# Performance work log

Hardware: AMD Instinct MI355X
Metric: run time of the kernel (lower is better)

## Reference

```python
import jax, jax.numpy as jnp
import numpy as np

D = 1024
H = 16
DH = D // H
FF = 4096
EPS = 1e-6


def setup_inputs() -> dict:
    key = jax.random.key(0)
    ks = jax.random.split(key, 8)
    s = 1.0 / np.sqrt(D)
    return {
        "x": jax.random.normal(ks[0], (2, 2048, D), jnp.float32),
        # attention projections stored [in, out] (math equals torch Linear x @ W.T)
        "w_q": jax.random.normal(ks[1], (D, D), jnp.float32) * s,
        "w_k": jax.random.normal(ks[2], (D, D), jnp.float32) * s,
        "w_v": jax.random.normal(ks[3], (D, D), jnp.float32) * s,
        "w_o": jax.random.normal(ks[4], (D, D), jnp.float32) * s,
        "w1": jax.random.normal(ks[5], (D, FF), jnp.float32) * s,
        "b1": jnp.zeros((FF,), jnp.float32),
        "w2": jax.random.normal(ks[6], (FF, D), jnp.float32) * (1.0 / np.sqrt(FF)),
        "b2": jnp.zeros((D,), jnp.float32),
        "g1": jnp.ones((D,), jnp.float32),
        "be1": jnp.zeros((D,), jnp.float32),
        "g2": jnp.ones((D,), jnp.float32),
        "be2": jnp.zeros((D,), jnp.float32),
    }


def _layernorm(x, gamma, beta):
    # torch .std() uses Bessel correction (ddof=1); note std+eps, not var+eps
    mean = jnp.mean(x, axis=-1, keepdims=True)
    std = jnp.std(x, axis=-1, keepdims=True, ddof=1)
    return gamma * (x - mean) / (std + EPS) + beta


def _attention(h, w_q, w_k, w_v, w_o):
    B, S, _ = h.shape
    q = (h @ w_q).reshape(B, S, H, DH)
    k = (h @ w_k).reshape(B, S, H, DH)
    v = (h @ w_v).reshape(B, S, H, DH)
    scores = jnp.einsum('bqhd,bkhd->bhqk', q, k) / np.sqrt(DH)  # [B,H,S,S]
    attn = jax.nn.softmax(scores, axis=-1)
    out = jnp.einsum('bhqk,bkhd->bqhd', attn, v).reshape(B, S, D)
    return out @ w_o


def reference(x, w_q, w_k, w_v, w_o, w1, b1, w2, b2, g1, be1, g2, be2):
    # pre-norm residual 1: self-attention (dropout=0 / eval)
    x = x + _attention(_layernorm(x, g1, be1), w_q, w_k, w_v, w_o)
    # pre-norm residual 2: FFN
    h = _layernorm(x, g2, be2)
    x = x + (jax.nn.relu(h @ w1 + b1) @ w2 + b2)
    return x
```

## Files before the change

### kernel.cpp

```cpp
#include <hip/hip_runtime.h>


typedef _Float16 half8 __attribute__((ext_vector_type(8)));
typedef _Float16 half4 __attribute__((ext_vector_type(4)));
typedef float floatx4 __attribute__((ext_vector_type(4)));

__device__ __forceinline__ void async16(const void* g, void* l) {
    __builtin_amdgcn_global_load_lds((const __attribute__((address_space(1))) unsigned int*)g,
                                     (__attribute__((address_space(3))) unsigned int*)l,
                                     16, 0, 0);
}

__global__ __launch_bounds__(256) void ln_kernel(const float* __restrict__ x,
                                                 const float* __restrict__ g,
                                                 const float* __restrict__ be,
                                                 _Float16* __restrict__ out) {
    int row = blockIdx.x;
    int tid = threadIdx.x;
    floatx4 v = ((const floatx4*)(x + (size_t)row * 1024))[tid];
    float s = 0.f, ss = 0.f;
#pragma unroll
    for (int i = 0; i < 4; i++) { s += v[i]; ss += v[i] * v[i]; }
#pragma unroll
    for (int off = 1; off < 64; off <<= 1) {
        s += __shfl_xor(s, off);
        ss += __shfl_xor(ss, off);
    }
    __shared__ float sm[8];
    int wave = tid >> 6, lane = tid & 63;
    if (lane == 0) { sm[wave] = s; sm[wave + 4] = ss; }
    __syncthreads();
    s = sm[0] + sm[1] + sm[2] + sm[3];
    ss = sm[4] + sm[5] + sm[6] + sm[7];
    float mean = s * (1.f / 1024.f);
    float var = (ss - s * mean) * (1.f / 1023.f);
    float rs = 1.f / (sqrtf(fmaxf(var, 0.f)) + 1e-6f);
    floatx4 gv = ((const floatx4*)g)[tid];
    floatx4 bv = ((const floatx4*)be)[tid];
    half4 o;
#pragma unroll
    for (int i = 0; i < 4; i++) o[i] = (_Float16)(gv[i] * (v[i] - mean) * rs + bv[i]);
    ((half4*)(out + (size_t)row * 1024))[tid] = o;
}

__global__ __launch_bounds__(256) void convt_kernel(const float* __restrict__ W, int ldW,
                                                    _Float16* __restrict__ WT, int Kr,
                                                    float scale) {
    __shared__ float t[64][65];
    int n0 = blockIdx.x * 64, k0 = blockIdx.y * 64;
    int tid = threadIdx.x;
    int r = tid >> 4, c4 = (tid & 15) * 4;
#pragma unroll
    for (int p = 0; p < 4; p++) {
        floatx4 v = *(const floatx4*)(W + (size_t)(k0 + r + p * 16) * ldW + n0 + c4);
#pragma unroll
        for (int j = 0; j < 4; j++) t[c4 + j][r + p * 16] = v[j];
    }
    __syncthreads();
#pragma unroll
    for (int p = 0; p < 4; p++) {
        int rr = r + p * 16;
        half4 o;
#pragma unroll
        for (int j = 0; j < 4; j++) o[j] = (_Float16)(t[rr][c4 + j] * scale);
        *(half4*)(WT + (size_t)(n0 + rr) * Kr + k0 + c4) = o;
    }
}

__global__ __launch_bounds__(256) void transv_kernel(const _Float16* __restrict__ V, int ldv,
                                                     _Float16* __restrict__ Vt) {
    __shared__ _Float16 t[64][72];
    int t0 = blockIdx.x * 64, d0 = blockIdx.y * 64;
    int tid = threadIdx.x;
#pragma unroll
    for (int i = 0; i < 2; i++) {
        int v = tid + i * 256;
        int r = v >> 3, c = (v & 7) * 8;
        half8 vv = *(const half8*)(V + (size_t)(t0 + r) * ldv + d0 + c);
#pragma unroll
        for (int j = 0; j < 8; j++) t[c + j][r] = vv[j];
    }
    __syncthreads();
    int bh = (t0 >> 11) * 16 + (d0 >> 6);
    int sbase = t0 & 2047;
#pragma unroll
    for (int i = 0; i < 2; i++) {
        int v = tid + i * 256;
        int r = v >> 3, c = (v & 7) * 8;
        half8 o = *(const half8*)&t[r][c];
        *(half8*)(Vt + ((size_t)bh * 64 + r) * 2048 + sbase + c) = o;
    }
}

__global__ __launch_bounds__(256) void gemm_t(const _Float16* __restrict__ A, int lda,
                                              const _Float16* __restrict__ BT,
                                              const float* __restrict__ bias,
                                              const float* res, void* Cout,
                                              int N, int K, int relu_flag, int out_fp16) {
    __shared__ _Float16 As[64 * 64];
    __shared__ _Float16 Bs[128 * 64];
    int tid = threadIdx.x;
    int wave = tid >> 6, lane = tid & 63, quad = lane >> 4, l15 = lane & 15;
    int bm = blockIdx.y * 64, bn = blockIdx.x * 128;
    int wr = (wave & 1) * 32, wc = (wave >> 1) * 64;
    int lrow = lane >> 3, lch = lane & 7;

    floatx4 acc[2][4];
#pragma unroll
    for (int im = 0; im < 2; im++)
#pragma unroll
        for (int in = 0; in < 4; in++)
#pragma unroll
            for (int r = 0; r < 4; r++) acc[im][in][r] = 0.f;

    for (int k0 = 0; k0 < K; k0 += 64) {
        __syncthreads();
#pragma unroll
        for (int ia = 0; ia < 2; ia++) {
            int g = 2 * wave + ia;
            int row = g * 8 + lrow;
            int ch = lch ^ (row & 7);
            async16(A + (size_t)(bm + row) * lda + k0 + ch * 8, &As[g * 512]);
        }
#pragma unroll
        for (int ib = 0; ib < 4; ib++) {
            int g = 4 * wave + ib;
            int row = g * 8 + lrow;
            int ch = lch ^ (row & 7);
            async16(BT + (size_t)(bn + row) * K + k0 + ch * 8, &Bs[g * 512]);
        }
        __syncthreads();

        half8 af[2][2], bf[4][2];
#pragma unroll
        for (int kk = 0; kk < 2; kk++) {
#pragma unroll
            for (int im = 0; im < 2; im++) {
                int m = wr + im * 16 + l15;
                af[im][kk] = *(const half8*)&As[m * 64 + ((((kk << 2) | quad) ^ (m & 7)) << 3)];
            }
#pragma unroll
            for (int in = 0; in < 4; in++) {
                int n = wc + in * 16 + l15;
                bf[in][kk] = *(const half8*)&Bs[n * 64 + ((((kk << 2) | quad) ^ (n & 7)) << 3)];
            }
        }
#pragma unroll
        for (int kk = 0; kk < 2; kk++)
#pragma unroll
            for (int im = 0; im < 2; im++)
#pragma unroll
                for (int in = 0; in < 4; in++)
                    acc[im][in] = __builtin_amdgcn_mfma_f32_16x16x32_f16(af[im][kk], bf[in][kk],
                                                                         acc[im][in], 0, 0, 0);
    }
#pragma unroll
    for (int im = 0; im < 2; im++)
#pragma unroll
        for (int in = 0; in < 4; in++)
#pragma unroll
            for (int r = 0; r < 4; r++) {
                int row = bm + wr + im * 16 + quad * 4 + r;
                int col = bn + wc + in * 16 + l15;
                float val = acc[im][in][r];
                if (bias) val += bias[col];
                if (relu_flag) val = fmaxf(val, 0.f);
                if (res) val += res[(size_t)row * N + col];
                if (out_fp16) ((_Float16*)Cout)[(size_t)row * N + col] = (_Float16)val;
                else          ((float*)Cout)[(size_t)row * N + col] = val;
            }
}

__global__ __launch_bounds__(256) void attn_kernel(const _Float16* Q,
                                                   const _Float16* __restrict__ K,
                                                   const _Float16* __restrict__ Vt,
                                                   _Float16* O, int ld) {
    __shared__ _Float16 Qs[64 * 64];
    __shared__ _Float16 KVs[2][2][64 * 64];
    int qt = blockIdx.x, bh = blockIdx.y;
    int b = bh >> 4, h = bh & 15;
    int col0 = h * 64, tbase = b * 2048;
    int tid = threadIdx.x;
    int wave = tid >> 6, lane = tid & 63, quad = lane >> 4, l15 = lane & 15;
    int lrow = lane >> 3, lch = lane & 7;

#pragma unroll
    for (int i = 0; i < 2; i++) {
        int g = 2 * wave + i;
        int row = g * 8 + lrow;
        int ch = lch ^ (row & 7);
        async16(Q + (size_t)(tbase + qt * 64 + row) * ld + col0 + ch * 8, &Qs[g * 512]);
        async16(K + (size_t)(tbase + row) * ld + col0 + ch * 8, &KVs[0][0][g * 512]);
        async16(Vt + ((size_t)bh * 64 + row) * 2048 + ch * 8, &KVs[0][1][g * 512]);
    }
    __syncthreads();

    int rowq = 16 * wave + l15;
    half8 bq[2];
#pragma unroll
    for (int kk = 0; kk < 2; kk++)
        bq[kk] = *(const half8*)&Qs[rowq * 64 + ((((kk << 2) | quad) ^ (rowq & 7)) << 3)];

    floatx4 o_acc[4];
#pragma unroll
    for (int im = 0; im < 4; im++)
#pragma unroll
        for (int r = 0; r < 4; r++) o_acc[im][r] = 0.f;
    float m_i = -1e30f, l_i = 0.f;

    for (int kt = 0; kt < 32; kt++) {
        if (kt) __syncthreads();
        if (kt + 1 < 32) {
            int nb = (kt + 1) & 1;
#pragma unroll
            for (int i = 0; i < 2; i++) {
                int g = 2 * wave + i;
                int row = g * 8 + lrow;
                int ch = lch ^ (row & 7);
                async16(K + (size_t)(tbase + (kt + 1) * 64 + row) * ld + col0 + ch * 8,
                        &KVs[nb][0][g * 512]);
                async16(Vt + ((size_t)bh * 64 + row) * 2048 + (kt + 1) * 64 + ch * 8,
                        &KVs[nb][1][g * 512]);
            }
        }
        const _Float16* Ks = KVs[kt & 1][0];
        const _Float16* Vs = KVs[kt & 1][1];

        floatx4 s_acc[4];
#pragma unroll
        for (int jn = 0; jn < 4; jn++)
#pragma unroll
            for (int r = 0; r < 4; r++) s_acc[jn][r] = 0.f;
#pragma unroll
        for (int jn = 0; jn < 4; jn++) {
            int rowk = 16 * jn + l15;
#pragma unroll
            for (int kk = 0; kk < 2; kk++) {
                half8 ak = *(const half8*)&Ks[rowk * 64 + ((((kk << 2) | quad) ^ (rowk & 7)) << 3)];
                s_acc[jn] = __builtin_amdgcn_mfma_f32_16x16x32_f16(ak, bq[kk], s_acc[jn], 0, 0, 0);
            }
        }

        float mx = -1e30f;
#pragma unroll
        for (int jn = 0; jn < 4; jn++)
#pragma unroll
            for (int r = 0; r < 4; r++) mx = fmaxf(mx, s_acc[jn][r]);
        mx = fmaxf(mx, __shfl_xor(mx, 16));
        mx = fmaxf(mx, __shfl_xor(mx, 32));
        float mnew = fmaxf(m_i, mx);
        float dd = m_i - mnew;
        float alpha = (dd < -60.f) ? 0.f : __expf(dd);
        m_i = mnew;

        float sum = 0.f;
#pragma unroll
        for (int jn = 0; jn < 4; jn++)
#pragma unroll
            for (int r = 0; r < 4; r++) {
                float d2 = s_acc[jn][r] - mnew;
                float p = (d2 < -60.f) ? 0.f : __expf(d2);
                s_acc[jn][r] = p;
                sum += p;
            }
        sum += __shfl_xor(sum, 16);
        sum += __shfl_xor(sum, 32);
        l_i = l_i * alpha + sum;

        half4 pb[4];
#pragma unroll
        for (int jn = 0; jn < 4; jn++)
#pragma unroll
            for (int r = 0; r < 4; r++) pb[jn][r] = (_Float16)s_acc[jn][r];

#pragma unroll
        for (int im = 0; im < 4; im++)
#pragma unroll
            for (int r = 0; r < 4; r++) o_acc[im][r] *= alpha;
#pragma unroll
        for (int im = 0; im < 4; im++) {
            int rowv = 16 * im + l15;
#pragma unroll
            for (int ks = 0; ks < 4; ks++) {
                int off = rowv * 128 + ((((2 * ks) | (quad >> 1)) ^ (rowv & 7)) << 4) + (quad & 1) * 8;
                half4 av = *(const half4*)((const char*)Vs + off);
                o_acc[im] = __builtin_amdgcn_mfma_f32_16x16x16f16(av, pb[ks], o_acc[im], 0, 0, 0);
            }
        }
    }

    float rl = 1.f / l_i;
#pragma unroll
    for (int im = 0; im < 4; im++) {
        half4 o;
#pragma unroll
        for (int r = 0; r < 4; r++) o[r] = (_Float16)(o_acc[im][r] * rl);
        *(half4*)&O[(size_t)(tbase + qt * 64 + wave * 16 + l15) * ld + col0 + im * 16 + quad * 4] = o;
    }
}

extern "C" void kernel_launch(void* const* d_in, const int* in_sizes, int n_in,
                              void* d_out, int out_size, void* d_ws, size_t ws_size,
                              hipStream_t stream) {
    const float* x   = (const float*)d_in[0];
    const float* wq  = (const float*)d_in[1];
    const float* wk  = (const float*)d_in[2];
    const float* wv  = (const float*)d_in[3];
    const float* wo  = (const float*)d_in[4];
    const float* w1  = (const float*)d_in[5];
    const float* b1  = (const float*)d_in[6];
    const float* w2  = (const float*)d_in[7];
    const float* b2  = (const float*)d_in[8];
    const float* g1  = (const float*)d_in[9];
    const float* be1 = (const float*)d_in[10];
    const float* g2  = (const float*)d_in[11];
    const float* be2 = (const float*)d_in[12];

    const size_t M1 = (size_t)1 << 20;
    _Float16* R0  = (_Float16*)d_ws;
    _Float16* QKV = R0 + 4 * M1;
    _Float16* R3  = R0 + 12 * M1;

    _Float16* wqkvT = (_Float16*)d_out;
    float* x1 = (float*)d_out;
    float* out = (float*)d_out;

    dim3 blk(256);

    convt_kernel<<<dim3(16, 16), blk, 0, stream>>>(wq, 1024, wqkvT, 1024, 0.125f);
    convt_kernel<<<dim3(16, 16), blk, 0, stream>>>(wk, 1024, wqkvT + (size_t)1024 * 1024, 1024, 1.f);
    convt_kernel<<<dim3(16, 16), blk, 0, stream>>>(wv, 1024, wqkvT + (size_t)2048 * 1024, 1024, 1.f);
    ln_kernel<<<4096, blk, 0, stream>>>(x, g1, be1, R0);
    gemm_t<<<dim3(24, 64), blk, 0, stream>>>(R0, 1024, wqkvT, nullptr, nullptr, QKV, 3072, 1024, 0, 1);
    transv_kernel<<<dim3(64, 16), blk, 0, stream>>>(QKV + 2048, 3072, R0);
    attn_kernel<<<dim3(32, 32), blk, 0, stream>>>(QKV, QKV + 1024, R0, QKV, 3072);
    convt_kernel<<<dim3(16, 16), blk, 0, stream>>>(wo, 1024, R0, 1024, 1.f);
    gemm_t<<<dim3(8, 64), blk, 0, stream>>>(QKV, 3072, R0, nullptr, x, x1, 1024, 1024, 0, 0);
    ln_kernel<<<4096, blk, 0, stream>>>(x1, g2, be2, R0);
    _Float16* f = QKV;
    for (int hh = 0; hh < 2; hh++) {
        _Float16* w1Th = R3;
        _Float16* w2Th = R3 + 2 * M1;
        convt_kernel<<<dim3(32, 16), blk, 0, stream>>>(w1 + hh * 2048, 4096, w1Th, 1024, 1.f);
        gemm_t<<<dim3(16, 64), blk, 0, stream>>>(R0, 1024, w1Th, b1 + hh * 2048, nullptr, f,
                                                 2048, 1024, 1, 1);
        convt_kernel<<<dim3(16, 32), blk, 0, stream>>>(w2 + (size_t)hh * 2048 * 1024, 1024, w2Th, 2048, 1.f);
        gemm_t<<<dim3(8, 64), blk, 0, stream>>>(f, 2048, w2Th, (hh == 1) ? b2 : nullptr, x1, out,
                                                1024, 2048, 0, 0);
    }
}
```

Measured before the change: 452.1 us.

## Add 128x128 GEMM tile for QKV/FFN1 and lazy-rescale online softmax in attention

Adds a gemm_t128 kernel with 128x128 output tiles (4x4 MFMA fragments per wave) and uses it for the QKV projection and the first FFN GEMM, raising arithmetic intensity per loaded tile. In attention, the running max is updated only when any lane's block max exceeds the current max by more than 8, which skips the rescale of O and l most of the time. Exponentials switch to exp2 with a folded log2e, and conversion uses packed round-toward-zero fp16. The new GEMM is single-buffered with more registers and fewer blocks, which may cost occupancy. The lazy max allows p values up to e^8, which fits in fp16 but loses a little precision.

```diff
diff --git a/kernel.cpp b/kernel.cpp
--- a/kernel.cpp
+++ b/kernel.cpp
@@ -3,6 +3,7 @@
 
 typedef _Float16 half8 __attribute__((ext_vector_type(8)));
 typedef _Float16 half4 __attribute__((ext_vector_type(4)));
+typedef __fp16 fp16x2 __attribute__((ext_vector_type(2)));
 typedef float floatx4 __attribute__((ext_vector_type(4)));
 
 __device__ __forceinline__ void async16(const void* g, void* l) {
@@ -171,6 +172,85 @@
             }
 }
 
+__global__ __launch_bounds__(256) void gemm_t128(const _Float16* __restrict__ A, int lda,
+                                                 const _Float16* __restrict__ BT,
+                                                 const float* __restrict__ bias,
+                                                 const float* res, void* Cout,
+                                                 int N, int K, int relu_flag, int out_fp16) {
+    __shared__ _Float16 As[128 * 64];
+    __shared__ _Float16 Bs[128 * 64];
+    int tid = threadIdx.x;
+    int wave = tid >> 6, lane = tid & 63, quad = lane >> 4, l15 = lane & 15;
+    int bm = blockIdx.y * 128, bn = blockIdx.x * 128;
+    int wr = (wave & 1) * 64, wc = (wave >> 1) * 64;
+    int lrow = lane >> 3, lch = lane & 7;
+
+    floatx4 acc[4][4];
+#pragma unroll
+    for (int im = 0; im < 4; im++)
+#pragma unroll
+        for (int in = 0; in < 4; in++)
+#pragma unroll
+            for (int r = 0; r < 4; r++) acc[im][in][r] = 0.f;
+
+    for (int k0 = 0; k0 < K; k0 += 64) {
+        __syncthreads();
+#pragma unroll
+        for (int ia = 0; ia < 4; ia++) {
+            int g = 4 * wave + ia;
+            int row = g * 8 + lrow;
+            int ch = lch ^ (row & 7);
+            async16(A + (size_t)(bm + row) * lda + k0 + ch * 8, &As[g * 512]);
+        }
+#pragma unroll
+        for (int ib = 0; ib < 4; ib++) {
+            int g = 4 * wave + ib;
+            int row = g * 8 + lrow;
+            int ch = lch ^ (row & 7);
+            async16(BT + (size_t)(bn + row) * K + k0 + ch * 8, &Bs[g * 512]);
+        }
+        __syncthreads();
+
+        half8 af[4][2], bf[4][2];
+#pragma unroll
+        for (int kk = 0; kk < 2; kk++) {
+#pragma unroll
+            for (int im = 0; im < 4; im++) {
+                int m = wr + im * 16 + l15;
+                af[im][kk] = *(const half8*)&As[m * 64 + ((((kk << 2) | quad) ^ (m & 7)) << 3)];
+            }
+#pragma unroll
+            for (int in = 0; in < 4; in++) {
+                int n = wc + in * 16 + l15;
+                bf[in][kk] = *(const half8*)&Bs[n * 64 + ((((kk << 2) | quad) ^ (n & 7)) << 3)];
+            }
+        }
+#pragma unroll
+        for (int kk = 0; kk < 2; kk++)
+#pragma unroll
+            for (int im = 0; im < 4; im++)
+#pragma unroll
+                for (int in = 0; in < 4; in++)
+                    acc[im][in] = __builtin_amdgcn_mfma_f32_16x16x32_f16(af[im][kk], bf[in][kk],
+                                                                         acc[im][in], 0, 0, 0);
+    }
+#pragma unroll
+    for (int im = 0; im < 4; im++)
+#pragma unroll
+        for (int in = 0; in < 4; in++)
+#pragma unroll
+            for (int r = 0; r < 4; r++) {
+                int row = bm + wr + im * 16 + quad * 4 + r;
+                int col = bn + wc + in * 16 + l15;
+                float val = acc[im][in][r];
+                if (bias) val += bias[col];
+                if (relu_flag) val = fmaxf(val, 0.f);
+                if (res) val += res[(size_t)row * N + col];
+                if (out_fp16) ((_Float16*)Cout)[(size_t)row * N + col] = (_Float16)val;
+                else          ((float*)Cout)[(size_t)row * N + col] = val;
+            }
+}
+
 __global__ __launch_bounds__(256) void attn_kernel(const _Float16* Q,
                                                    const _Float16* __restrict__ K,
                                                    const _Float16* __restrict__ Vt,
@@ -207,6 +287,7 @@
 #pragma unroll
         for (int r = 0; r < 4; r++) o_acc[im][r] = 0.f;
     float m_i = -1e30f, l_i = 0.f;
+    const float LOG2E = 1.44269504f;
 
     for (int kt = 0; kt < 32; kt++) {
         if (kt) __syncthreads();
@@ -248,35 +329,37 @@
             for (int r = 0; r < 4; r++) mx = fmaxf(mx, s_acc[jn][r]);
         mx = fmaxf(mx, __shfl_xor(mx, 16));
         mx = fmaxf(mx, __shfl_xor(mx, 32));
-        float mnew = fmaxf(m_i, mx);
-        float dd = m_i - mnew;
-        float alpha = (dd < -60.f) ? 0.f : __expf(dd);
-        m_i = mnew;
+        if (!__all(mx <= m_i + 8.f)) {
+            float mnew = fmaxf(m_i, mx);
+            float dd = m_i - mnew;
+            float alpha = (dd < -60.f) ? 0.f : __expf(dd);
+            l_i *= alpha;
+#pragma unroll
+            for (int im = 0; im < 4; im++)
+#pragma unroll
+                for (int r = 0; r < 4; r++) o_acc[im][r] *= alpha;
+            m_i = mnew;
+        }
+        float m2 = m_i * LOG2E;
 
         float sum = 0.f;
-#pragma unroll
-        for (int jn = 0; jn < 4; jn++)
-#pragma unroll
-            for (int r = 0; r < 4; r++) {
-                float d2 = s_acc[jn][r] - mnew;
-                float p = (d2 < -60.f) ? 0.f : __expf(d2);
-                s_acc[jn][r] = p;
-                sum += p;
-            }
+        half4 pb[4];
+#pragma unroll
+        for (int jn = 0; jn < 4; jn++) {
+            float p0 = exp2f(fmaf(s_acc[jn][0], LOG2E, -m2));
+            float p1 = exp2f(fmaf(s_acc[jn][1], LOG2E, -m2));
+            float p2 = exp2f(fmaf(s_acc[jn][2], LOG2E, -m2));
+            float p3 = exp2f(fmaf(s_acc[jn][3], LOG2E, -m2));
+            sum += (p0 + p1) + (p2 + p3);
+            fp16x2 lo = __builtin_amdgcn_cvt_pkrtz(p0, p1);
+            fp16x2 hi = __builtin_amdgcn_cvt_pkrtz(p2, p3);
+            pb[jn][0] = (_Float16)lo[0]; pb[jn][1] = (_Float16)lo[1];
+            pb[jn][2] = (_Float16)hi[0]; pb[jn][3] = (_Float16)hi[1];
+        }
         sum += __shfl_xor(sum, 16);
         sum += __shfl_xor(sum, 32);
-        l_i = l_i * alpha + sum;
-
-        half4 pb[4];
-#pragma unroll
-        for (int jn = 0; jn < 4; jn++)
-#pragma unroll
-            for (int r = 0; r < 4; r++) pb[jn][r] = (_Float16)s_acc[jn][r];
-
-#pragma unroll
-        for (int im = 0; im < 4; im++)
-#pragma unroll
-            for (int r = 0; r < 4; r++) o_acc[im][r] *= alpha;
+        l_i += sum;
+
 #pragma unroll
         for (int im = 0; im < 4; im++) {
             int rowv = 16 * im + l15;
@@ -331,7 +414,7 @@
     convt_kernel<<<dim3(16, 16), blk, 0, stream>>>(wk, 1024, wqkvT + (size_t)1024 * 1024, 1024, 1.f);
     convt_kernel<<<dim3(16, 16), blk, 0, stream>>>(wv, 1024, wqkvT + (size_t)2048 * 1024, 1024, 1.f);
     ln_kernel<<<4096, blk, 0, stream>>>(x, g1, be1, R0);
-    gemm_t<<<dim3(24, 64), blk, 0, stream>>>(R0, 1024, wqkvT, nullptr, nullptr, QKV, 3072, 1024, 0, 1);
+    gemm_t128<<<dim3(24, 32), blk, 0, stream>>>(R0, 1024, wqkvT, nullptr, nullptr, QKV, 3072, 1024, 0, 1);
     transv_kernel<<<dim3(64, 16), blk, 0, stream>>>(QKV + 2048, 3072, R0);
     attn_kernel<<<dim3(32, 32), blk, 0, stream>>>(QKV, QKV + 1024, R0, QKV, 3072);
     convt_kernel<<<dim3(16, 16), blk, 0, stream>>>(wo, 1024, R0, 1024, 1.f);
@@ -342,8 +425,8 @@
         _Float16* w1Th = R3;
         _Float16* w2Th = R3 + 2 * M1;
         convt_kernel<<<dim3(32, 16), blk, 0, stream>>>(w1 + hh * 2048, 4096, w1Th, 1024, 1.f);
-        gemm_t<<<dim3(16, 64), blk, 0, stream>>>(R0, 1024, w1Th, b1 + hh * 2048, nullptr, f,
-                                                 2048, 1024, 1, 1);
+        gemm_t128<<<dim3(16, 32), blk, 0, stream>>>(R0, 1024, w1Th, b1 + hh * 2048, nullptr, f,
+                                                    2048, 1024, 1, 1);
         convt_kernel<<<dim3(16, 32), blk, 0, stream>>>(w2 + (size_t)hh * 2048 * 1024, 1024, w2Th, 2048, 1.f);
         gemm_t<<<dim3(8, 64), blk, 0, stream>>>(f, 2048, w2Th, (hh == 1) ? b2 : nullptr, x1, out,
                                                 1024, 2048, 0, 0);
```

Measured after the change: 461.5 us. +2.1%, slower.

## Unroll attention loop by two with precomputed LDS pointers and lazy rescaling

Applied to the files above, without the earlier changes.

Restructures the flash-attention inner loop into a two-step unrolled body with compile-time buffer indices, precomputed LDS fragment pointers and incrementing global pointers, to cut per-iteration address arithmetic. It also adds a lazy online-softmax rescale that skips the alpha correction unless the max grows by more than a threshold, uses exp2 with a fused log2e scale, and packs fp16 conversion with cvt_pkrtz. Keeping many precomputed pointers raises register pressure. Skipping the rescale lets p values reach up to e^8 before normalisation, and round-toward-zero conversion slightly changes rounding.

```diff
diff --git a/kernel.cpp b/kernel.cpp
--- a/kernel.cpp
+++ b/kernel.cpp
@@ -3,6 +3,7 @@
 
 typedef _Float16 half8 __attribute__((ext_vector_type(8)));
 typedef _Float16 half4 __attribute__((ext_vector_type(4)));
+typedef __fp16 fp16x2 __attribute__((ext_vector_type(2)));
 typedef float floatx4 __attribute__((ext_vector_type(4)));
 
 __device__ __forceinline__ void async16(const void* g, void* l) {
@@ -171,6 +172,71 @@
             }
 }
 
+template <int BUF>
+__device__ __forceinline__ void attn_step(const half8* const (&kfp)[2][4][2],
+                                          const half4* const (&vfp)[2][4][4],
+                                          const half8 (&bq)[2],
+                                          floatx4 (&o_acc)[4],
+                                          float& m_i, float& l_i) {
+    const float LOG2E = 1.44269504f;
+    floatx4 s_acc[4];
+#pragma unroll
+    for (int jn = 0; jn < 4; jn++)
+#pragma unroll
+        for (int r = 0; r < 4; r++) s_acc[jn][r] = 0.f;
+#pragma unroll
+    for (int jn = 0; jn < 4; jn++)
+#pragma unroll
+        for (int kk = 0; kk < 2; kk++)
+            s_acc[jn] = __builtin_amdgcn_mfma_f32_16x16x32_f16(*kfp[BUF][jn][kk], bq[kk],
+                                                               s_acc[jn], 0, 0, 0);
+
+    float mx = -1e30f;
+#pragma unroll
+    for (int jn = 0; jn < 4; jn++)
+#pragma unroll
+        for (int r = 0; r < 4; r++) mx = fmaxf(mx, s_acc[jn][r]);
+    mx = fmaxf(mx, __shfl_xor(mx, 16));
+    mx = fmaxf(mx, __shfl_xor(mx, 32));
+    if (!__all(mx <= m_i + 8.f)) {
+        float mnew = fmaxf(m_i, mx);
+        float dd = m_i - mnew;
+        float alpha = (dd < -60.f) ? 0.f : __expf(dd);
+        l_i *= alpha;
+#pragma unroll
+        for (int im = 0; im < 4; im++)
+#pragma unroll
+            for (int r = 0; r < 4; r++) o_acc[im][r] *= alpha;
+        m_i = mnew;
+    }
+    float m2 = m_i * LOG2E;
+
+    float sum = 0.f;
+    half4 pb[4];
+#pragma unroll
+    for (int jn = 0; jn < 4; jn++) {
+        float p0 = exp2f(fmaf(s_acc[jn][0], LOG2E, -m2));
+        float p1 = exp2f(fmaf(s_acc[jn][1], LOG2E, -m2));
+        float p2 = exp2f(fmaf(s_acc[jn][2], LOG2E, -m2));
+        float p3 = exp2f(fmaf(s_acc[jn][3], LOG2E, -m2));
+        sum += (p0 + p1) + (p2 + p3);
+        fp16x2 lo = __builtin_amdgcn_cvt_pkrtz(p0, p1);
+        fp16x2 hi = __builtin_amdgcn_cvt_pkrtz(p2, p3);
+        pb[jn][0] = (_Float16)lo[0]; pb[jn][1] = (_Float16)lo[1];
+        pb[jn][2] = (_Float16)hi[0]; pb[jn][3] = (_Float16)hi[1];
+    }
+    sum += __shfl_xor(sum, 16);
+    sum += __shfl_xor(sum, 32);
+    l_i += sum;
+
+#pragma unroll
+    for (int im = 0; im < 4; im++)
+#pragma unroll
+        for (int ks = 0; ks < 4; ks++)
+            o_acc[im] = __builtin_amdgcn_mfma_f32_16x16x16f16(*vfp[BUF][im][ks], pb[ks],
+                                                              o_acc[im], 0, 0, 0);
+}
+
 __global__ __launch_bounds__(256) void attn_kernel(const _Float16* Q,
                                                    const _Float16* __restrict__ K,
                                                    const _Float16* __restrict__ Vt,
@@ -184,14 +250,21 @@
     int wave = tid >> 6, lane = tid & 63, quad = lane >> 4, l15 = lane & 15;
     int lrow = lane >> 3, lch = lane & 7;
 
+    const _Float16* kg[2];
+    const _Float16* vg[2];
+    const size_t kadv = (size_t)64 * ld;
 #pragma unroll
     for (int i = 0; i < 2; i++) {
         int g = 2 * wave + i;
         int row = g * 8 + lrow;
         int ch = lch ^ (row & 7);
+        kg[i] = K + (size_t)(tbase + row) * ld + col0 + ch * 8;
+        vg[i] = Vt + ((size_t)bh * 64 + row) * 2048 + ch * 8;
         async16(Q + (size_t)(tbase + qt * 64 + row) * ld + col0 + ch * 8, &Qs[g * 512]);
-        async16(K + (size_t)(tbase + row) * ld + col0 + ch * 8, &KVs[0][0][g * 512]);
-        async16(Vt + ((size_t)bh * 64 + row) * 2048 + ch * 8, &KVs[0][1][g * 512]);
+        async16(kg[i], &KVs[0][0][g * 512]);
+        async16(vg[i], &KVs[0][1][g * 512]);
+        kg[i] += kadv;
+        vg[i] += 64;
     }
     __syncthreads();
 
@@ -201,6 +274,30 @@
     for (int kk = 0; kk < 2; kk++)
         bq[kk] = *(const half8*)&Qs[rowq * 64 + ((((kk << 2) | quad) ^ (rowq & 7)) << 3)];
 
+    const half8* kfp[2][4][2];
+    const half4* vfp[2][4][4];
+#pragma unroll
+    for (int bb = 0; bb < 2; bb++) {
+#pragma unroll
+        for (int jn = 0; jn < 4; jn++) {
+            int rowk = 16 * jn + l15;
+#pragma unroll
+            for (int kk = 0; kk < 2; kk++)
+                kfp[bb][jn][kk] = (const half8*)
+                    &KVs[bb][0][rowk * 64 + ((((kk << 2) | quad) ^ (rowk & 7)) << 3)];
+        }
+#pragma unroll
+        for (int im = 0; im < 4; im++) {
+            int rowv = 16 * im + l15;
+#pragma unroll
+            for (int ks = 0; ks < 4; ks++) {
+                int off = rowv * 128 + ((((2 * ks) | (quad >> 1)) ^ (rowv & 7)) << 4)
+                          + (quad & 1) * 8;
+                vfp[bb][im][ks] = (const half4*)((const char*)KVs[bb][1] + off);
+            }
+        }
+    }
+
     floatx4 o_acc[4];
 #pragma unroll
     for (int im = 0; im < 4; im++)
@@ -208,85 +305,29 @@
         for (int r = 0; r < 4; r++) o_acc[im][r] = 0.f;
     float m_i = -1e30f, l_i = 0.f;
 
-    for (int kt = 0; kt < 32; kt++) {
-        if (kt) __syncthreads();
-        if (kt + 1 < 32) {
-            int nb = (kt + 1) & 1;
+#pragma unroll 1
+    for (int kt2 = 0; kt2 < 16; kt2++) {
+        if (kt2) __syncthreads();
+#pragma unroll
+        for (int i = 0; i < 2; i++) {
+            async16(kg[i], &KVs[1][0][(2 * wave + i) * 512]);
+            async16(vg[i], &KVs[1][1][(2 * wave + i) * 512]);
+            kg[i] += kadv;
+            vg[i] += 64;
+        }
+        attn_step<0>(kfp, vfp, bq, o_acc, m_i, l_i);
+
+        __syncthreads();
+        if (kt2 < 15) {
 #pragma unroll
             for (int i = 0; i < 2; i++) {
-                int g = 2 * wave + i;
-                int row = g * 8 + lrow;
-                int ch = lch ^ (row & 7);
-                async16(K + (size_t)(tbase + (kt + 1) * 64 + row) * ld + col0 + ch * 8,
-                        &KVs[nb][0][g * 512]);
-                async16(Vt + ((size_t)bh * 64 + row) * 2048 + (kt + 1) * 64 + ch * 8,
-                        &KVs[nb][1][g * 512]);
-            }
-        }
-        const _Float16* Ks = KVs[kt & 1][0];
-        const _Float16* Vs = KVs[kt & 1][1];
-
-        floatx4 s_acc[4];
-#pragma unroll
-        for (int jn = 0; jn < 4; jn++)
-#pragma unroll
-            for (int r = 0; r < 4; r++) s_acc[jn][r] = 0.f;
-#pragma unroll
-        for (int jn = 0; jn < 4; jn++) {
-            int rowk = 16 * jn + l15;
-#pragma unroll
-            for (int kk = 0; kk < 2; kk++) {
-                half8 ak = *(const half8*)&Ks[rowk * 64 + ((((kk << 2) | quad) ^ (rowk & 7)) << 3)];
-                s_acc[jn] = __builtin_amdgcn_mfma_f32_16x16x32_f16(ak, bq[kk], s_acc[jn], 0, 0, 0);
-            }
-        }
-
-        float mx = -1e30f;
-#pragma unroll
-        for (int jn = 0; jn < 4; jn++)
-#pragma unroll
-            for (int r = 0; r < 4; r++) mx = fmaxf(mx, s_acc[jn][r]);
-        mx = fmaxf(mx, __shfl_xor(mx, 16));
-        mx = fmaxf(mx, __shfl_xor(mx, 32));
-        float mnew = fmaxf(m_i, mx);
-        float dd = m_i - mnew;
-        float alpha = (dd < -60.f) ? 0.f : __expf(dd);
-        m_i = mnew;
-
-        float sum = 0.f;
-#pragma unroll
-        for (int jn = 0; jn < 4; jn++)
-#pragma unroll
-            for (int r = 0; r < 4; r++) {
-                float d2 = s_acc[jn][r] - mnew;
-                float p = (d2 < -60.f) ? 0.f : __expf(d2);
-                s_acc[jn][r] = p;
-                sum += p;
-            }
-        sum += __shfl_xor(sum, 16);
-        sum += __shfl_xor(sum, 32);
-        l_i = l_i * alpha + sum;
-
-        half4 pb[4];
-#pragma unroll
-        for (int jn = 0; jn < 4; jn++)
-#pragma unroll
-            for (int r = 0; r < 4; r++) pb[jn][r] = (_Float16)s_acc[jn][r];
-
-#pragma unroll
-        for (int im = 0; im < 4; im++)
-#pragma unroll
-            for (int r = 0; r < 4; r++) o_acc[im][r] *= alpha;
-#pragma unroll
-        for (int im = 0; im < 4; im++) {
-            int rowv = 16 * im + l15;
-#pragma unroll
-            for (int ks = 0; ks < 4; ks++) {
-                int off = rowv * 128 + ((((2 * ks) | (quad >> 1)) ^ (rowv & 7)) << 4) + (quad & 1) * 8;
-                half4 av = *(const half4*)((const char*)Vs + off);
-                o_acc[im] = __builtin_amdgcn_mfma_f32_16x16x16f16(av, pb[ks], o_acc[im], 0, 0, 0);
-            }
-        }
+                async16(kg[i], &KVs[0][0][(2 * wave + i) * 512]);
+                async16(vg[i], &KVs[0][1][(2 * wave + i) * 512]);
+                kg[i] += kadv;
+                vg[i] += 64;
+            }
+        }
+        attn_step<1>(kfp, vfp, bq, o_acc, m_i, l_i);
     }
 
     float rl = 1.f / l_i;
```

New measurement: 465.3 us. 1.03x slower.
